# Optimization experiments

Hardware: AMD Instinct MI355X
Metric: run time of the kernel (lower is better)

The kernel has to match this reference:

```python
import jax, jax.numpy as jnp
import numpy as np

H = 768          # hidden_size
NH = 12          # num heads
HD = H // NH     # head dim
NEG = -1e9       # stand-in for -inf masked_fill (numerically safe)


def setup_inputs() -> dict:
    key = jax.random.key(0)
    ks = jax.random.split(key, 8)
    B, T = 4, 2048
    s = 0.02
    return {
        "hidden_states": jax.random.normal(ks[0], (B, T, H), jnp.float32),
        "attention_mask": jnp.zeros((B, 1, 1, T), jnp.float32),
        "Wq": jax.random.normal(ks[1], (H, H), jnp.float32) * s,
        "bq": jnp.zeros((H,), jnp.float32),
        "Wk": jax.random.normal(ks[2], (H, H), jnp.float32) * s,
        "bk": jnp.zeros((H,), jnp.float32),
        "Wv": jax.random.normal(ks[3], (H, H), jnp.float32) * s,
        "bv": jnp.zeros((H,), jnp.float32),
    }


def _split_heads(x):
    b, t, _ = x.shape
    return x.reshape(b, t, NH, HD).transpose(0, 2, 1, 3)  # b h t d


def reference(hidden_states, attention_mask, Wq, bq, Wk, bk, Wv, bv):
    q = _split_heads(hidden_states @ Wq.T + bq)
    k = _split_heads(hidden_states @ Wk.T + bk)
    v = _split_heads(hidden_states @ Wv.T + bv)
    T = q.shape[2]
    scores = jnp.einsum('bhid,bhjd->bhij', q, k) / jnp.sqrt(jnp.float32(HD))
    causal = jnp.tril(jnp.ones((T, T), bool))
    scores = jnp.where(causal, scores, NEG) + attention_mask
    probs = jax.nn.softmax(scores, axis=-1)
    out = jnp.einsum('bhij,bhjd->bhid', probs, v)
    b = out.shape[0]
    return out.transpose(0, 2, 1, 3).reshape(b, T, H)  # b t (h d)
```

## Files before the change

kernel.cpp:

```cpp
#include <hip/hip_runtime.h>
#include <hip/hip_bf16.h>

#define Tsz 2048
#define Hsz 768
#define NHsz 12
#define HDsz 64

typedef unsigned short u16;
typedef unsigned int u32;
typedef __attribute__((ext_vector_type(8))) short bf16x8;
typedef __attribute__((ext_vector_type(4))) float f32x4;
typedef __attribute__((ext_vector_type(4))) u16 u16x4;

__device__ __forceinline__ u16 f2bf(float f) {
    union { __hip_bfloat16 h; u16 u; } c;
    c.h = __float2bfloat16(f);
    return c.u;
}

__device__ __forceinline__ void glds16(const void* src, void* ldsbase) {
    __builtin_amdgcn_global_load_lds(
        (const __attribute__((address_space(1))) u32*)src,
        (__attribute__((address_space(3))) u32*)ldsbase, 16, 0, 0);
}

#define BAR() do { asm volatile("" ::: "memory"); \
                   __builtin_amdgcn_s_barrier();  \
                   asm volatile("" ::: "memory"); } while (0)

#define LDSFRAG(base, row, c) \
    (*(const bf16x8*)((const char*)(base) + (row)*128 + ((((c) << 4)) ^ (((row) & 7) << 4))))

__global__ __launch_bounds__(256) void qkv_mfma(
    const float* __restrict__ X,
    const float* __restrict__ Wq, const float* __restrict__ bq,
    const float* __restrict__ Wk, const float* __restrict__ bk,
    const float* __restrict__ Wv, const float* __restrict__ bv,
    u16* __restrict__ q_ws, u16* __restrict__ k_ws, u16* __restrict__ vt_ws)
{
    const int tid = threadIdx.x;
    const int w = tid >> 6, l = tid & 63, lg = l >> 4, lh = l & 15;
    const int m0 = blockIdx.x * 128;
    const int nb = blockIdx.y;
    const int z = nb / 6;
    const int n0l = (nb % 6) * 128;
    const float* W    = (z == 0) ? Wq : (z == 1) ? Wk : Wv;
    const float* bias = (z == 0) ? bq : (z == 1) ? bk : bv;

    __shared__ __align__(16) u16 Xs[128 * 64];
    __shared__ __align__(16) u16 Ws[128 * 64];

    const int wm = w >> 1, wn = w & 1;

    f32x4 acc[4][4];
    #pragma unroll
    for (int i = 0; i < 4; ++i)
        #pragma unroll
        for (int j = 0; j < 4; ++j)
            acc[i][j] = (f32x4){0.f, 0.f, 0.f, 0.f};

    for (int k0 = 0; k0 < Hsz; k0 += 64) {
        __syncthreads();
        #pragma unroll
        for (int p = 0; p < 4; ++p) {
            int id = tid + p * 256;
            int r = id >> 3, c8 = id & 7;
            int cswz = c8 ^ (r & 7);
            float4 xa = *(const float4*)(X + (size_t)(m0 + r) * Hsz + k0 + c8 * 8);
            float4 xb = *(const float4*)(X + (size_t)(m0 + r) * Hsz + k0 + c8 * 8 + 4);
            bf16x8 xv;
            xv[0] = (short)f2bf(xa.x); xv[1] = (short)f2bf(xa.y);
            xv[2] = (short)f2bf(xa.z); xv[3] = (short)f2bf(xa.w);
            xv[4] = (short)f2bf(xb.x); xv[5] = (short)f2bf(xb.y);
            xv[6] = (short)f2bf(xb.z); xv[7] = (short)f2bf(xb.w);
            *(bf16x8*)((char*)Xs + r * 128 + cswz * 16) = xv;
            float4 wa = *(const float4*)(W + (size_t)(n0l + r) * Hsz + k0 + c8 * 8);
            float4 wb = *(const float4*)(W + (size_t)(n0l + r) * Hsz + k0 + c8 * 8 + 4);
            bf16x8 wv8;
            wv8[0] = (short)f2bf(wa.x); wv8[1] = (short)f2bf(wa.y);
            wv8[2] = (short)f2bf(wa.z); wv8[3] = (short)f2bf(wa.w);
            wv8[4] = (short)f2bf(wb.x); wv8[5] = (short)f2bf(wb.y);
            wv8[6] = (short)f2bf(wb.z); wv8[7] = (short)f2bf(wb.w);
            *(bf16x8*)((char*)Ws + r * 128 + cswz * 16) = wv8;
        }
        __syncthreads();
        #pragma unroll
        for (int s = 0; s < 2; ++s) {
            bf16x8 af[4], bfr[4];
            #pragma unroll
            for (int tq = 0; tq < 4; ++tq) {
                af[tq]  = LDSFRAG(Xs, wm * 64 + tq * 16 + lh, 4 * s + lg);
                bfr[tq] = LDSFRAG(Ws, wn * 64 + tq * 16 + lh, 4 * s + lg);
            }
            #pragma unroll
            for (int mt = 0; mt < 4; ++mt)
                #pragma unroll
                for (int nt = 0; nt < 4; ++nt)
                    acc[mt][nt] = __builtin_amdgcn_mfma_f32_16x16x32_bf16(
                        af[mt], bfr[nt], acc[mt][nt], 0, 0, 0);
        }
    }

    #pragma unroll
    for (int nt = 0; nt < 4; ++nt) {
        int nloc = n0l + wn * 64 + nt * 16 + lh;
        float bval = bias[nloc];
        int hh = nloc >> 6, d = nloc & 63;
        #pragma unroll
        for (int mt = 0; mt < 4; ++mt) {
            #pragma unroll
            for (int r = 0; r < 4; ++r) {
                int m = m0 + wm * 64 + mt * 16 + lg * 4 + r;
                int bb = m >> 11, t = m & 2047;
                u16 val = f2bf(acc[mt][nt][r] + bval);
                size_t bh = (size_t)(bb * NHsz + hh);
                if (z == 0)      q_ws[(bh * Tsz + t) * HDsz + d] = val;
                else if (z == 1) k_ws[(bh * Tsz + t) * HDsz + d] = val;
                else             vt_ws[(bh * HDsz + d) * Tsz + t] = val;
            }
        }
    }
}

__global__ __launch_bounds__(256) void attn_mfma(
    const u16* __restrict__ q_ws, const u16* __restrict__ k_ws,
    const u16* __restrict__ vt_ws, const float* __restrict__ am,
    float* __restrict__ out)
{
    const int tid = threadIdx.x;
    const int w = tid >> 6, l = tid & 63, lg = l >> 4, lh = l & 15;
    const int bx = blockIdx.x;
    const int h = blockIdx.y, b = blockIdx.z;
    const int bh = b * NHsz + h;

    const u16* Qb = q_ws + (size_t)bh * Tsz * HDsz;
    const u16* Kb = k_ws + (size_t)bh * Tsz * HDsz;
    const u16* Vb = vt_ws + (size_t)bh * HDsz * Tsz;
    const float* amb = am + (size_t)b * Tsz;

    __shared__ __align__(16) u16 Ks[2][64 * 64];
    __shared__ __align__(16) u16 Vs[2][64 * 64];
    __shared__ __align__(16) u16 Ps[4][16 * 64];
    __shared__ __align__(16) float ambs[Tsz];

    const float LOG2E  = 1.44269504f;
    const float SCALE2 = 0.125f * 1.44269504f;
    const f32x4 zero4 = {0.f, 0.f, 0.f, 0.f};
    u16* myP = &Ps[w][0];
    const int srcbase = l & 0x30;
    const int qo = lg * 4;

    #pragma unroll
    for (int i = 0; i < 2; ++i)
        glds16(amb + (size_t)(i * 256 + tid) * 4, ambs + (i * 256 + w * 64) * 4);
    asm volatile("s_waitcnt vmcnt(0)" ::: "memory");
    __syncthreads();
    #pragma unroll
    for (int i = 0; i < 8; ++i) ambs[tid * 8 + i] *= LOG2E;
    __syncthreads();

    #pragma unroll 1
    for (int ph = 0; ph < 2; ++ph) {
        const int qt = (ph == 0) ? (16 + bx) : (15 - bx);
        const int q0 = qt * 64 + w * 16;
        const int qrow = q0 + lh;

        #pragma unroll
        for (int p = 0; p < 2; ++p) {
            int id = w * 128 + p * 64 + l;
            int r = id >> 3, c8 = id & 7;
            int cswz = c8 ^ (r & 7);
            glds16(Kb + (size_t)r * HDsz + cswz * 8, &Ks[0][(w * 128 + p * 64) * 8]);
            glds16(Vb + (size_t)r * Tsz + cswz * 8, &Vs[0][(w * 128 + p * 64) * 8]);
        }
        bf16x8 qf0 = *(const bf16x8*)(Qb + (size_t)(q0 + lh) * HDsz + lg * 8);
        bf16x8 qf1 = *(const bf16x8*)(Qb + (size_t)(q0 + lh) * HDsz + lg * 8 + 32);
        asm volatile("s_waitcnt vmcnt(0)" ::: "memory");
        BAR();

        f32x4 o[4];
        #pragma unroll
        for (int n = 0; n < 4; ++n) o[n] = zero4;
        float m2 = -1e30f, l2 = 0.f;

        #pragma unroll 1
        for (int kt = 0; kt <= qt; ++kt) {
            const int cur = kt & 1;
            const int kv0 = kt * 64;

            if (kt < qt) {
                const int kv1 = kv0 + 64;
                #pragma unroll
                for (int p = 0; p < 2; ++p) {
                    int id = w * 128 + p * 64 + l;
                    int r = id >> 3, c8 = id & 7;
                    int cswz = c8 ^ (r & 7);
                    glds16(Kb + (size_t)(kv1 + r) * HDsz + cswz * 8,
                           &Ks[cur ^ 1][(w * 128 + p * 64) * 8]);
                    glds16(Vb + (size_t)r * Tsz + kv1 + cswz * 8,
                           &Vs[cur ^ 1][(w * 128 + p * 64) * 8]);
                }
                asm volatile("s_waitcnt vmcnt(4)" ::: "memory");
            } else {
                asm volatile("s_waitcnt vmcnt(0)" ::: "memory");
            }
            BAR();

            const u16* Ksb = &Ks[cur][0];
            const u16* Vsb = &Vs[cur][0];
            const bool diag = (kt == qt);

            f32x4 st[4];
            __builtin_amdgcn_s_setprio(1);
            if (!diag) {
                #pragma unroll
                for (int n = 0; n < 4; ++n) {
                    int row = n * 16 + lh;
                    bf16x8 kf0 = LDSFRAG(Ksb, row, lg);
                    bf16x8 kf1 = LDSFRAG(Ksb, row, 4 + lg);
                    f32x4 c = __builtin_amdgcn_mfma_f32_16x16x32_bf16(kf0, qf0, zero4, 0, 0, 0);
                    st[n] = __builtin_amdgcn_mfma_f32_16x16x32_bf16(kf1, qf1, c, 0, 0, 0);
                }
            } else {
                #pragma unroll
                for (int n = 0; n < 4; ++n) {
                    st[n] = zero4;
                    if (n <= w) {
                        int row = n * 16 + lh;
                        bf16x8 kf0 = LDSFRAG(Ksb, row, lg);
                        bf16x8 kf1 = LDSFRAG(Ksb, row, 4 + lg);
                        f32x4 c = __builtin_amdgcn_mfma_f32_16x16x32_bf16(kf0, qf0, zero4, 0, 0, 0);
                        st[n] = __builtin_amdgcn_mfma_f32_16x16x32_bf16(kf1, qf1, c, 0, 0, 0);
                    }
                }
            }
            __builtin_amdgcn_s_setprio(0);

            float pvv[16];
            float mx = -1e30f;
            if (!diag) {
                #pragma unroll
                for (int n = 0; n < 4; ++n) {
                    f32x4 a4 = *(const f32x4*)(ambs + kv0 + n * 16 + lg * 4);
                    #pragma unroll
                    for (int r = 0; r < 4; ++r) {
                        float sv = fmaf(st[n][r], SCALE2, a4[r]);
                        pvv[n * 4 + r] = sv;
                        mx = fmaxf(mx, sv);
                    }
                }
            } else {
                #pragma unroll
                for (int n = 0; n < 4; ++n) {
                    f32x4 a4 = *(const f32x4*)(ambs + kv0 + n * 16 + lg * 4);
                    #pragma unroll
                    for (int r = 0; r < 4; ++r) {
                        int kvj = kv0 + n * 16 + lg * 4 + r;
                        float sv = (kvj > qrow) ? -1e30f : fmaf(st[n][r], SCALE2, a4[r]);
                        pvv[n * 4 + r] = sv;
                        mx = fmaxf(mx, sv);
                    }
                }
            }
            mx = fmaxf(mx, __shfl_xor(mx, 16));
            mx = fmaxf(mx, __shfl_xor(mx, 32));

            const bool norescale = __all(mx <= m2 + 8.0f);
            float mn = m2;
            if (!norescale) mn = fmaxf(m2, mx);

            float ps = 0.f;
            #pragma unroll
            for (int i = 0; i < 16; ++i) {
                float p = exp2f(pvv[i] - mn);
                pvv[i] = p;
                ps += p;
            }
            ps += __shfl_xor(ps, 16);
            ps += __shfl_xor(ps, 32);

            if (norescale) {
                l2 += ps;
            } else {
                float corr = exp2f(m2 - mn);
                m2 = mn;
                l2 = l2 * corr + ps;
                float co[4];
                #pragma unroll
                for (int r = 0; r < 4; ++r)
                    co[r] = __shfl(corr, srcbase | (qo + r));
                #pragma unroll
                for (int n = 0; n < 4; ++n)
                    #pragma unroll
                    for (int r = 0; r < 4; ++r)
                        o[n][r] *= co[r];
            }

            #pragma unroll
            for (int n = 0; n < 4; ++n) {
                u16x4 v;
                v[0] = f2bf(pvv[n * 4 + 0]); v[1] = f2bf(pvv[n * 4 + 1]);
                v[2] = f2bf(pvv[n * 4 + 2]); v[3] = f2bf(pvv[n * 4 + 3]);
                int chunk = 2 * n + (lg >> 1);
                int byteoff = lh * 128 + ((chunk ^ (lh & 7)) << 4) + ((lg & 1) << 3);
                *(u16x4*)((char*)myP + byteoff) = v;
            }

            const int smaxv = (diag && w < 2) ? 0 : 1;
            __builtin_amdgcn_s_setprio(1);
            #pragma unroll
            for (int s = 0; s < 2; ++s) {
                if (s <= smaxv) {
                    int chunk = (4 * s + lg) ^ (lh & 7);
                    bf16x8 pf = *(const bf16x8*)((const char*)myP + lh * 128 + (chunk << 4));
                    #pragma unroll
                    for (int n = 0; n < 4; ++n) {
                        bf16x8 vf = LDSFRAG(Vsb, n * 16 + lh, 4 * s + lg);
                        o[n] = __builtin_amdgcn_mfma_f32_16x16x32_bf16(pf, vf, o[n], 0, 0, 0);
                    }
                }
            }
            __builtin_amdgcn_s_setprio(0);
            BAR();
        }

        float linv[4];
        #pragma unroll
        for (int r = 0; r < 4; ++r)
            linv[r] = 1.0f / __shfl(l2, srcbase | (qo + r));
        float* ob = out + ((size_t)(b * Tsz + q0 + qo)) * Hsz + h * HDsz + lh;
        #pragma unroll
        for (int r = 0; r < 4; ++r)
            #pragma unroll
            for (int n = 0; n < 4; ++n)
                ob[r * Hsz + n * 16] = o[n][r] * linv[r];
    }
}

extern "C" void kernel_launch(void* const* d_in, const int* in_sizes, int n_in,
                              void* d_out, int out_size, void* d_ws, size_t ws_size,
                              hipStream_t stream) {
    const float* X  = (const float*)d_in[0];
    const float* am = (const float*)d_in[1];
    const float* Wq = (const float*)d_in[2];
    const float* bq = (const float*)d_in[3];
    const float* Wk = (const float*)d_in[4];
    const float* bk = (const float*)d_in[5];
    const float* Wv = (const float*)d_in[6];
    const float* bv = (const float*)d_in[7];
    float* out = (float*)d_out;

    const size_t per = (size_t)8192 * Hsz;
    u16* q_ws  = (u16*)d_ws;
    u16* k_ws  = q_ws + per;
    u16* vt_ws = k_ws + per;

    dim3 g1(64, 18);
    qkv_mfma<<<g1, 256, 0, stream>>>(X, Wq, bq, Wk, bk, Wv, bv, q_ws, k_ws, vt_ws);

    dim3 g2(16, NHsz, 4);
    attn_mfma<<<g2, 256, 0, stream>>>(q_ws, k_ws, vt_ws, am, out);
}
```

Baseline: 163.1 us.

## Pre-convert inputs to bf16 and double-buffer QKV GEMM with async LDS loads

Adds a separate kernel that converts X and the three weight matrices to bf16 once, using the output buffer as scratch. The QKV GEMM then streams bf16 tiles straight into double-buffered LDS with global_load_lds, overlapping the next tile's loads with the current MFMAs, raises wave priority during compute, and swaps grid order so the N blocks for one M tile run together. This removes the redundant fp32 loads and conversions that were repeated in every block, at the cost of an extra launch plus a write and reread of bf16 data.

```diff
diff --git a/kernel.cpp b/kernel.cpp
--- a/kernel.cpp
+++ b/kernel.cpp
@@ -31,24 +31,56 @@
 #define LDSFRAG(base, row, c) \
     (*(const bf16x8*)((const char*)(base) + (row)*128 + ((((c) << 4)) ^ (((row) & 7) << 4))))
 
-__global__ __launch_bounds__(256) void qkv_mfma(
+__global__ __launch_bounds__(256) void to_bf16(
     const float* __restrict__ X,
-    const float* __restrict__ Wq, const float* __restrict__ bq,
-    const float* __restrict__ Wk, const float* __restrict__ bk,
-    const float* __restrict__ Wv, const float* __restrict__ bv,
+    const float* __restrict__ Wq, const float* __restrict__ Wk,
+    const float* __restrict__ Wv,
+    u16* __restrict__ xb, u16* __restrict__ wb)
+{
+    const int bx = blockIdx.x, tid = threadIdx.x;
+    const float* src;
+    u16* dst;
+    size_t off;
+    if (bx < 768) {
+        src = X; dst = xb;
+        off = ((size_t)bx * 256 + tid) * 32;
+    } else {
+        int r = bx - 768;
+        int wsel = r / 72, lr = r % 72;
+        src = (wsel == 0) ? Wq : (wsel == 1) ? Wk : Wv;
+        dst = wb + (size_t)wsel * (Hsz * Hsz);
+        off = ((size_t)lr * 256 + tid) * 32;
+    }
+    #pragma unroll
+    for (int c = 0; c < 4; ++c) {
+        float4 a = *(const float4*)(src + off + c * 8);
+        float4 b = *(const float4*)(src + off + c * 8 + 4);
+        bf16x8 v;
+        v[0] = (short)f2bf(a.x); v[1] = (short)f2bf(a.y);
+        v[2] = (short)f2bf(a.z); v[3] = (short)f2bf(a.w);
+        v[4] = (short)f2bf(b.x); v[5] = (short)f2bf(b.y);
+        v[6] = (short)f2bf(b.z); v[7] = (short)f2bf(b.w);
+        *(bf16x8*)(dst + off + c * 8) = v;
+    }
+}
+
+__global__ __launch_bounds__(256) void qkv_gemm(
+    const u16* __restrict__ xb, const u16* __restrict__ wb,
+    const float* __restrict__ bq, const float* __restrict__ bk,
+    const float* __restrict__ bv,
     u16* __restrict__ q_ws, u16* __restrict__ k_ws, u16* __restrict__ vt_ws)
 {
     const int tid = threadIdx.x;
     const int w = tid >> 6, l = tid & 63, lg = l >> 4, lh = l & 15;
-    const int m0 = blockIdx.x * 128;
-    const int nb = blockIdx.y;
+    const int nb = blockIdx.x;
+    const int m0 = blockIdx.y * 128;
     const int z = nb / 6;
     const int n0l = (nb % 6) * 128;
-    const float* W    = (z == 0) ? Wq : (z == 1) ? Wk : Wv;
+    const u16* Wb = wb + (size_t)z * (Hsz * Hsz);
     const float* bias = (z == 0) ? bq : (z == 1) ? bk : bv;
 
-    __shared__ __align__(16) u16 Xs[128 * 64];
-    __shared__ __align__(16) u16 Ws[128 * 64];
+    __shared__ __align__(16) u16 Xs[2][128 * 64];
+    __shared__ __align__(16) u16 Ws[2][128 * 64];
 
     const int wm = w >> 1, wn = w & 1;
 
@@ -59,38 +91,42 @@
         for (int j = 0; j < 4; ++j)
             acc[i][j] = (f32x4){0.f, 0.f, 0.f, 0.f};
 
-    for (int k0 = 0; k0 < Hsz; k0 += 64) {
-        __syncthreads();
+    auto stage = [&](int buf, int k0) {
         #pragma unroll
         for (int p = 0; p < 4; ++p) {
-            int id = tid + p * 256;
+            int id = w * 256 + p * 64 + l;
             int r = id >> 3, c8 = id & 7;
             int cswz = c8 ^ (r & 7);
-            float4 xa = *(const float4*)(X + (size_t)(m0 + r) * Hsz + k0 + c8 * 8);
-            float4 xb = *(const float4*)(X + (size_t)(m0 + r) * Hsz + k0 + c8 * 8 + 4);
-            bf16x8 xv;
-            xv[0] = (short)f2bf(xa.x); xv[1] = (short)f2bf(xa.y);
-            xv[2] = (short)f2bf(xa.z); xv[3] = (short)f2bf(xa.w);
-            xv[4] = (short)f2bf(xb.x); xv[5] = (short)f2bf(xb.y);
-            xv[6] = (short)f2bf(xb.z); xv[7] = (short)f2bf(xb.w);
-            *(bf16x8*)((char*)Xs + r * 128 + cswz * 16) = xv;
-            float4 wa = *(const float4*)(W + (size_t)(n0l + r) * Hsz + k0 + c8 * 8);
-            float4 wb = *(const float4*)(W + (size_t)(n0l + r) * Hsz + k0 + c8 * 8 + 4);
-            bf16x8 wv8;
-            wv8[0] = (short)f2bf(wa.x); wv8[1] = (short)f2bf(wa.y);
-            wv8[2] = (short)f2bf(wa.z); wv8[3] = (short)f2bf(wa.w);
-            wv8[4] = (short)f2bf(wb.x); wv8[5] = (short)f2bf(wb.y);
-            wv8[6] = (short)f2bf(wb.z); wv8[7] = (short)f2bf(wb.w);
-            *(bf16x8*)((char*)Ws + r * 128 + cswz * 16) = wv8;
-        }
-        __syncthreads();
+            glds16(xb + (size_t)(m0 + r) * Hsz + k0 + cswz * 8,
+                   &Xs[buf][(w * 256 + p * 64) * 8]);
+            glds16(Wb + (size_t)(n0l + r) * Hsz + k0 + cswz * 8,
+                   &Ws[buf][(w * 256 + p * 64) * 8]);
+        }
+    };
+
+    stage(0, 0);
+    asm volatile("s_waitcnt vmcnt(0)" ::: "memory");
+    BAR();
+
+    #pragma unroll 1
+    for (int ks = 0; ks < 12; ++ks) {
+        const int cur = ks & 1;
+        if (ks < 11) {
+            stage(cur ^ 1, (ks + 1) * 64);
+            asm volatile("s_waitcnt vmcnt(8)" ::: "memory");
+        } else {
+            asm volatile("s_waitcnt vmcnt(0)" ::: "memory");
+        }
+        BAR();
+
+        __builtin_amdgcn_s_setprio(1);
         #pragma unroll
         for (int s = 0; s < 2; ++s) {
             bf16x8 af[4], bfr[4];
             #pragma unroll
             for (int tq = 0; tq < 4; ++tq) {
-                af[tq]  = LDSFRAG(Xs, wm * 64 + tq * 16 + lh, 4 * s + lg);
-                bfr[tq] = LDSFRAG(Ws, wn * 64 + tq * 16 + lh, 4 * s + lg);
+                af[tq]  = LDSFRAG(Xs[cur], wm * 64 + tq * 16 + lh, 4 * s + lg);
+                bfr[tq] = LDSFRAG(Ws[cur], wn * 64 + tq * 16 + lh, 4 * s + lg);
             }
             #pragma unroll
             for (int mt = 0; mt < 4; ++mt)
@@ -99,6 +135,8 @@
                     acc[mt][nt] = __builtin_amdgcn_mfma_f32_16x16x32_bf16(
                         af[mt], bfr[nt], acc[mt][nt], 0, 0, 0);
         }
+        __builtin_amdgcn_s_setprio(0);
+        BAR();
     }
 
     #pragma unroll
@@ -355,8 +393,13 @@
     u16* k_ws  = q_ws + per;
     u16* vt_ws = k_ws + per;
 
-    dim3 g1(64, 18);
-    qkv_mfma<<<g1, 256, 0, stream>>>(X, Wq, bq, Wk, bk, Wv, bv, q_ws, k_ws, vt_ws);
+    u16* xb = (u16*)d_out;
+    u16* wb = xb + per;
+
+    to_bf16<<<dim3(984), 256, 0, stream>>>(X, Wq, Wk, Wv, xb, wb);
+
+    dim3 g1(18, 64);
+    qkv_gemm<<<g1, 256, 0, stream>>>(xb, wb, bq, bk, bv, q_ws, k_ws, vt_ws);
 
     dim3 g2(16, NHsz, 4);
     attn_mfma<<<g2, 256, 0, stream>>>(q_ws, k_ws, vt_ws, am, out);
```

After: 150.3 us. 7.8% less time.
